# Performance work log

Measured on AMD Instinct MI355X. Metric: run time of the kernel, lower is better.

## Reference

```python
import jax, jax.numpy as jnp
import numpy as np

N = 8192
BOX = 50.0
CUTOFF = 5.0
MAX_E = 64 * N  # padded edge capacity (~34 avg neighbors expected)


def setup_inputs() -> dict:
    key = jax.random.key(0)
    pos = jax.random.uniform(key, (N, 3), dtype=jnp.float32) * BOX
    return {"pos": pos}


def _pairwise_dist(pos):
    # Euclidean cdist via the gram-matrix identity; avoids the [N,N,3] intermediate.
    sq = jnp.sum(pos * pos, axis=-1)                      # [N]
    d2 = sq[:, None] + sq[None, :] - 2.0 * (pos @ pos.T)  # [N,N]
    return jnp.sqrt(jnp.maximum(d2, 0.0))


def reference(pos):
    n = pos.shape[0]
    dist = _pairwise_dist(pos)
    # mask self-edges by pushing the diagonal above the cutoff (as in the torch code)
    dist = dist + (CUTOFF + 1.0) * jnp.eye(n, dtype=dist.dtype)
    mask = dist < CUTOFF
    # data-dependent nonzero -> fixed-size padded output for jit compatibility;
    # padded entries are filled with -1.
    rows, cols = jnp.nonzero(mask, size=MAX_E, fill_value=-1)
    return jnp.stack([rows, cols], axis=0)  # [2, MAX_E], int32
```

## Files before the change

### kernel.cpp

```cpp
#include <hip/hip_runtime.h>
#include <stdint.h>

#define N 8192
#define MAX_E (64 * N)
#define NCHUNK (N / 64)
#define TILE 2048
#define A_ROWS_PER_WAVE 4
#define A_WAVES 4
#define A_ROWS_PER_BLOCK (A_ROWS_PER_WAVE * A_WAVES)
#define A_NBLOCKS (N / A_ROWS_PER_BLOCK)

__device__ __forceinline__ float sq_exact(float x, float y, float z) {
    return __fadd_rn(__fadd_rn(__fmul_rn(x, x), __fmul_rn(y, y)), __fmul_rn(z, z));
}

__device__ __forceinline__ bool edge_pred(float xi, float yi, float zi, float sqi,
                                          const float4& pj) {
    float dot = __fmaf_rn(zi, pj.z, __fmaf_rn(yi, pj.y, __fmul_rn(xi, pj.x)));
    float d2  = __fmaf_rn(-2.0f, dot, __fadd_rn(sqi, pj.w));
    return d2 < 0x1.8ffffep+4f;
}

__global__ __launch_bounds__(256) void mask_kernel(const float* __restrict__ posf,
                                                   uint64_t* __restrict__ masks,
                                                   int* __restrict__ counts) {
    __shared__ float4 pts[TILE];
    const int tid  = threadIdx.x;
    const int wave = tid >> 6;
    const int lane = tid & 63;
    const int row0 = blockIdx.x * A_ROWS_PER_BLOCK + wave * A_ROWS_PER_WAVE;

    float xi[A_ROWS_PER_WAVE], yi[A_ROWS_PER_WAVE], zi[A_ROWS_PER_WAVE], sqi[A_ROWS_PER_WAVE];
    uint64_t k0[A_ROWS_PER_WAVE], k1[A_ROWS_PER_WAVE];
#pragma unroll
    for (int r = 0; r < A_ROWS_PER_WAVE; r++) {
        int i = row0 + r;
        xi[r] = posf[3 * i + 0];
        yi[r] = posf[3 * i + 1];
        zi[r] = posf[3 * i + 2];
        sqi[r] = sq_exact(xi[r], yi[r], zi[r]);
        k0[r] = 0; k1[r] = 0;
    }

    for (int tb = 0; tb < N; tb += TILE) {
        __syncthreads();
        for (int k = tid; k < TILE; k += 256) {
            float x = posf[3 * (tb + k) + 0];
            float y = posf[3 * (tb + k) + 1];
            float z = posf[3 * (tb + k) + 2];
            pts[k] = make_float4(x, y, z, sq_exact(x, y, z));
        }
        __syncthreads();
#pragma unroll 4
        for (int c = 0; c < TILE; c += 128) {
            const int owner = ((tb + c) >> 7) & 63;
            float4 pa = pts[c + lane];
            float4 pb = pts[c + 64 + lane];
#pragma unroll
            for (int r = 0; r < A_ROWS_PER_WAVE; r++) {
                uint64_t ma = __ballot(edge_pred(xi[r], yi[r], zi[r], sqi[r], pa));
                if (lane == owner) k0[r] = ma;
                uint64_t mb = __ballot(edge_pred(xi[r], yi[r], zi[r], sqi[r], pb));
                if (lane == owner) k1[r] = mb;
            }
        }
    }

#pragma unroll
    for (int r = 0; r < A_ROWS_PER_WAVE; r++) {
        const int row = row0 + r;
        const int gs = row >> 6;
        if (lane == (gs >> 1)) {
            uint64_t clr = ~(1ull << (row & 63));
            if (gs & 1) k1[r] &= clr; else k0[r] &= clr;
        }
        ulonglong2 v; v.x = k0[r]; v.y = k1[r];
        ((ulonglong2*)(masks + (size_t)row * NCHUNK))[lane] = v;
        int t = __popcll(k0[r]) + __popcll(k1[r]);
#pragma unroll
        for (int o = 32; o > 0; o >>= 1) t += __shfl_down(t, o);
        if (lane == 0) counts[row] = t;
    }
}

__global__ __launch_bounds__(256) void scan_kernel(const int* __restrict__ counts,
                                                   int* __restrict__ offsets) {
    __shared__ int part[256];
    const int t = threadIdx.x;
    int local[32];
    int s = 0;
#pragma unroll
    for (int k = 0; k < 32; k++) { local[k] = counts[t * 32 + k]; s += local[k]; }
    part[t] = s;
    __syncthreads();
    for (int off = 1; off < 256; off <<= 1) {
        int v = (t >= off) ? part[t - off] : 0;
        __syncthreads();
        part[t] += v;
        __syncthreads();
    }
    int run = (t > 0) ? part[t - 1] : 0;
#pragma unroll
    for (int k = 0; k < 32; k++) { offsets[t * 32 + k] = run; run += local[k]; }
    if (t == 255) offsets[N] = part[255];
}

__global__ __launch_bounds__(256) void emit_kernel(const uint64_t* __restrict__ masks,
                                                   const int* __restrict__ offsets,
                                                   int* __restrict__ out) {
    const int wave = threadIdx.x >> 6;
    const int lane = threadIdx.x & 63;
    const int row  = blockIdx.x * 4 + wave;

    {
        const int E = offsets[N];
        const int idx = E + blockIdx.x * 256 + threadIdx.x;
        if (idx < MAX_E) { out[idx] = -1; out[MAX_E + idx] = -1; }
    }

    ulonglong2 v = ((const ulonglong2*)(masks + (size_t)row * NCHUNK))[lane];
    int s0 = __popcll(v.x), s1 = __popcll(v.y);
    int x = s0 + s1;
#pragma unroll
    for (int o = 1; o < 64; o <<= 1) {
        int t = __shfl_up(x, o);
        if (lane >= o) x += t;
    }
    int slot = offsets[row] + (x - (s0 + s1));

    const int col0 = lane * 128;
    uint64_t m = v.x;
    while (m) {
        int b = __ffsll((unsigned long long)m) - 1;
        m &= m - 1;
        if (slot < MAX_E) { out[slot] = row; out[MAX_E + slot] = col0 + b; }
        slot++;
    }
    m = v.y;
    while (m) {
        int b = __ffsll((unsigned long long)m) - 1;
        m &= m - 1;
        if (slot < MAX_E) { out[slot] = row; out[MAX_E + slot] = col0 + 64 + b; }
        slot++;
    }
}

extern "C" void kernel_launch(void* const* d_in, const int* in_sizes, int n_in,
                              void* d_out, int out_size, void* d_ws, size_t ws_size,
                              hipStream_t stream) {
    const float* posf = (const float*)d_in[0];
    int* out = (int*)d_out;
    int* counts  = (int*)d_ws;
    int* offsets = counts + N;
    uint64_t* masks = (uint64_t*)((char*)d_ws + (128 << 10));

    mask_kernel<<<A_NBLOCKS, 256, 0, stream>>>(posf, masks, counts);
    scan_kernel<<<1, 256, 0, stream>>>(counts, offsets);
    emit_kernel<<<N / 4, 256, 0, stream>>>(masks, offsets, out);
}
```

Before: 87.69 us.

## Split mask kernel across column tiles via 2D grid with per-tile counts

The mask kernel now launches a 2D grid (row groups × 8 column tiles of 1024), so each block handles a single column tile instead of looping over all 8192 columns. This raises the block count from 512 to 4096 and shortens each block's serial loop, which should improve occupancy and latency hiding across CUs. Per-row counts become per-(row, tile) partial counts that the single-block scan kernel has to sum, adding reads to that serial stage. Each block also reloads the row positions and a smaller tile, adding some redundant global traffic.

Measured after the change: 94.21 us. 7.4% more time.

```diff
diff --git a/kernel.cpp b/kernel.cpp
--- a/kernel.cpp
+++ b/kernel.cpp
@@ -4,11 +4,12 @@
 #define N 8192
 #define MAX_E (64 * N)
 #define NCHUNK (N / 64)
-#define TILE 2048
-#define A_ROWS_PER_WAVE 4
-#define A_WAVES 4
-#define A_ROWS_PER_BLOCK (A_ROWS_PER_WAVE * A_WAVES)
-#define A_NBLOCKS (N / A_ROWS_PER_BLOCK)
+#define TILE 1024
+#define CTILES (N / TILE)
+#define ROWS_PER_WAVE 4
+#define WAVES 4
+#define ROWS_PER_BLOCK (ROWS_PER_WAVE * WAVES)
+#define RGROUPS (N / ROWS_PER_BLOCK)
 
 __device__ __forceinline__ float sq_exact(float x, float y, float z) {
     return __fadd_rn(__fadd_rn(__fmul_rn(x, x), __fmul_rn(y, y)), __fmul_rn(z, z));
@@ -23,17 +24,19 @@
 
 __global__ __launch_bounds__(256) void mask_kernel(const float* __restrict__ posf,
                                                    uint64_t* __restrict__ masks,
-                                                   int* __restrict__ counts) {
+                                                   int* __restrict__ counts8) {
     __shared__ float4 pts[TILE];
     const int tid  = threadIdx.x;
     const int wave = tid >> 6;
     const int lane = tid & 63;
-    const int row0 = blockIdx.x * A_ROWS_PER_BLOCK + wave * A_ROWS_PER_WAVE;
+    const int row0 = blockIdx.x * ROWS_PER_BLOCK + wave * ROWS_PER_WAVE;
+    const int ct   = blockIdx.y;
+    const int cb   = ct * TILE;
 
-    float xi[A_ROWS_PER_WAVE], yi[A_ROWS_PER_WAVE], zi[A_ROWS_PER_WAVE], sqi[A_ROWS_PER_WAVE];
-    uint64_t k0[A_ROWS_PER_WAVE], k1[A_ROWS_PER_WAVE];
+    float xi[ROWS_PER_WAVE], yi[ROWS_PER_WAVE], zi[ROWS_PER_WAVE], sqi[ROWS_PER_WAVE];
+    uint64_t k0[ROWS_PER_WAVE], k1[ROWS_PER_WAVE];
 #pragma unroll
-    for (int r = 0; r < A_ROWS_PER_WAVE; r++) {
+    for (int r = 0; r < ROWS_PER_WAVE; r++) {
         int i = row0 + r;
         xi[r] = posf[3 * i + 0];
         yi[r] = posf[3 * i + 1];
@@ -42,55 +45,62 @@
         k0[r] = 0; k1[r] = 0;
     }
 
-    for (int tb = 0; tb < N; tb += TILE) {
-        __syncthreads();
-        for (int k = tid; k < TILE; k += 256) {
-            float x = posf[3 * (tb + k) + 0];
-            float y = posf[3 * (tb + k) + 1];
-            float z = posf[3 * (tb + k) + 2];
-            pts[k] = make_float4(x, y, z, sq_exact(x, y, z));
-        }
-        __syncthreads();
-#pragma unroll 4
-        for (int c = 0; c < TILE; c += 128) {
-            const int owner = ((tb + c) >> 7) & 63;
-            float4 pa = pts[c + lane];
-            float4 pb = pts[c + 64 + lane];
+    for (int k = tid; k < TILE; k += 256) {
+        float x = posf[3 * (cb + k) + 0];
+        float y = posf[3 * (cb + k) + 1];
+        float z = posf[3 * (cb + k) + 2];
+        pts[k] = make_float4(x, y, z, sq_exact(x, y, z));
+    }
+    __syncthreads();
+
 #pragma unroll
-            for (int r = 0; r < A_ROWS_PER_WAVE; r++) {
-                uint64_t ma = __ballot(edge_pred(xi[r], yi[r], zi[r], sqi[r], pa));
-                if (lane == owner) k0[r] = ma;
-                uint64_t mb = __ballot(edge_pred(xi[r], yi[r], zi[r], sqi[r], pb));
-                if (lane == owner) k1[r] = mb;
-            }
+    for (int c = 0; c < TILE; c += 128) {
+        const int owner = c >> 7;
+        float4 pa = pts[c + lane];
+        float4 pb = pts[c + 64 + lane];
+#pragma unroll
+        for (int r = 0; r < ROWS_PER_WAVE; r++) {
+            uint64_t ma = __ballot(edge_pred(xi[r], yi[r], zi[r], sqi[r], pa));
+            if (lane == owner) k0[r] = ma;
+            uint64_t mb = __ballot(edge_pred(xi[r], yi[r], zi[r], sqi[r], pb));
+            if (lane == owner) k1[r] = mb;
         }
     }
 
 #pragma unroll
-    for (int r = 0; r < A_ROWS_PER_WAVE; r++) {
+    for (int r = 0; r < ROWS_PER_WAVE; r++) {
         const int row = row0 + r;
-        const int gs = row >> 6;
-        if (lane == (gs >> 1)) {
-            uint64_t clr = ~(1ull << (row & 63));
-            if (gs & 1) k1[r] &= clr; else k0[r] &= clr;
+        if ((row >> 10) == ct) {
+            const int ls = (row & (TILE - 1)) >> 6;
+            if (lane == (ls >> 1)) {
+                uint64_t clr = ~(1ull << (row & 63));
+                if (ls & 1) k1[r] &= clr; else k0[r] &= clr;
+            }
         }
-        ulonglong2 v; v.x = k0[r]; v.y = k1[r];
-        ((ulonglong2*)(masks + (size_t)row * NCHUNK))[lane] = v;
+        if (lane < CTILES) {
+            ulonglong2 v; v.x = k0[r]; v.y = k1[r];
+            ((ulonglong2*)(masks + (size_t)row * NCHUNK))[ct * (TILE / 128) + lane] = v;
+        }
         int t = __popcll(k0[r]) + __popcll(k1[r]);
 #pragma unroll
         for (int o = 32; o > 0; o >>= 1) t += __shfl_down(t, o);
-        if (lane == 0) counts[row] = t;
+        if (lane == 0) counts8[row * CTILES + ct] = t;
     }
 }
 
-__global__ __launch_bounds__(256) void scan_kernel(const int* __restrict__ counts,
+__global__ __launch_bounds__(256) void scan_kernel(const int* __restrict__ counts8,
                                                    int* __restrict__ offsets) {
     __shared__ int part[256];
     const int t = threadIdx.x;
     int local[32];
     int s = 0;
 #pragma unroll
-    for (int k = 0; k < 32; k++) { local[k] = counts[t * 32 + k]; s += local[k]; }
+    for (int k = 0; k < 32; k++) {
+        int v = 0;
+#pragma unroll
+        for (int j = 0; j < CTILES; j++) v += counts8[(t * 32 + k) * CTILES + j];
+        local[k] = v; s += v;
+    }
     part[t] = s;
     __syncthreads();
     for (int off = 1; off < 256; off <<= 1) {
@@ -150,11 +160,12 @@
                               hipStream_t stream) {
     const float* posf = (const float*)d_in[0];
     int* out = (int*)d_out;
-    int* counts  = (int*)d_ws;
-    int* offsets = counts + N;
-    uint64_t* masks = (uint64_t*)((char*)d_ws + (128 << 10));
+    int* counts8 = (int*)d_ws;
+    int* offsets = (int*)((char*)d_ws + (256 << 10));
+    uint64_t* masks = (uint64_t*)((char*)d_ws + (512 << 10));
 
-    mask_kernel<<<A_NBLOCKS, 256, 0, stream>>>(posf, masks, counts);
-    scan_kernel<<<1, 256, 0, stream>>>(counts, offsets);
+    dim3 grid(RGROUPS, CTILES);
+    mask_kernel<<<grid, 256, 0, stream>>>(posf, masks, counts8);
+    scan_kernel<<<1, 256, 0, stream>>>(counts8, offsets);
     emit_kernel<<<N / 4, 256, 0, stream>>>(masks, offsets, out);
 }
```
